# Optimization experiments

Hardware: AMD Instinct MI355X
Metric: run time of the kernel (lower is better)

Reference implementation:

```python
import jax, jax.numpy as jnp
import numpy as np

B, S, D, H = 4, 2048, 1024, 16
DK = D // H


def setup_inputs() -> dict:
    key = jax.random.key(0)
    ks = jax.random.split(key, 5)
    scale = 1.0 / np.sqrt(D)
    return {
        "x": jax.random.normal(ks[0], (B, S, D), dtype=jnp.float32),
        "mask": jnp.ones((1, 1, S, S), dtype=bool),
        "Wq": jax.random.normal(ks[1], (D, D), dtype=jnp.float32) * scale,
        "Wk": jax.random.normal(ks[2], (D, D), dtype=jnp.float32) * scale,
        "Wv": jax.random.normal(ks[3], (D, D), dtype=jnp.float32) * scale,
        "Wo": jax.random.normal(ks[4], (D, D), dtype=jnp.float32) * scale,
    }


def reference(x, mask, Wq, Wk, Wv, Wo):
    # nn.Linear(d_model, d_model, bias=False): y = x @ W.T
    q = jnp.einsum('bsd,ed->bse', x, Wq).reshape(B, S, H, DK).transpose(0, 2, 1, 3)
    k = jnp.einsum('bsd,ed->bse', x, Wk).reshape(B, S, H, DK).transpose(0, 2, 1, 3)
    v = jnp.einsum('bsd,ed->bse', x, Wv).reshape(B, S, H, DK).transpose(0, 2, 1, 3)
    # scaled dot-product attention: [B,H,S,S]
    scores = jnp.einsum('bhqd,bhkd->bhqk', q, k) / jnp.sqrt(jnp.float32(DK))
    scores = jnp.where(mask, scores, jnp.float32(-1e9))
    attn = jax.nn.softmax(scores, axis=-1)
    out = jnp.einsum('bhqk,bhkd->bhqd', attn, v)  # [B,H,S,DK]
    out = out.transpose(0, 2, 1, 3).reshape(B, S, D)
    return jnp.einsum('bsd,ed->bse', out, Wo)
```

## Files before the change

### kernel.cpp

```cpp
#include <hip/hip_runtime.h>

typedef __bf16 bf16x8 __attribute__((ext_vector_type(8)));
typedef float f32x4 __attribute__((ext_vector_type(4)));
typedef float f32x16 __attribute__((ext_vector_type(16)));
typedef unsigned short u16;
typedef unsigned short u16x8 __attribute__((ext_vector_type(8)));
typedef unsigned short u16x4 __attribute__((ext_vector_type(4)));
typedef unsigned int u32;
typedef unsigned int u32x4 __attribute__((ext_vector_type(4)));

#define MFMA16(a, b, c) __builtin_amdgcn_mfma_f32_16x16x32_bf16(a, b, c, 0, 0, 0)
#define MFMA32(a, b, c) __builtin_amdgcn_mfma_f32_32x32x16_bf16(a, b, c, 0, 0, 0)

#if defined(__has_builtin)
#if __has_builtin(__builtin_amdgcn_exp2f)
#define EXP2(x) __builtin_amdgcn_exp2f(x)
#endif
#endif
#ifndef EXP2
#define EXP2(x) exp2f(x)
#endif

constexpr int NB = 4, NH = 16, SEQ = 2048, DM = 1024, DKH = 64;
constexpr int MTOT = NB * SEQ;
constexpr size_t QKV_ELEMS = (size_t)MTOT * DM;
constexpr size_t W_ELEMS = (size_t)DM * DM;
constexpr float QSCALE = 0.125f * 1.44269504088896340736f;

__device__ __forceinline__ int swz(int row, int col, int rowlen) {
  return (row * rowlen + col) ^ ((row & 7) << 3);
}

__device__ __forceinline__ void gload16(const u16* g, u16* l) {
  __builtin_amdgcn_global_load_lds(
      (const __attribute__((address_space(1))) void*)g,
      (__attribute__((address_space(3))) void*)l, 16, 0, 0);
}

__device__ __forceinline__ u32 cvtpk(float lo, float hi) {
  u32 r;
  asm("v_cvt_pk_bf16_f32 %0, %1, %2" : "=v"(r) : "v"(lo), "v"(hi));
  return r;
}
__device__ __forceinline__ void plswap(u32& a, u32& b) {
  asm volatile("v_permlane32_swap_b32 %0, %1" : "+v"(a), "+v"(b));
}

__global__ __launch_bounds__(256) void convert_bf16(
    const float* __restrict__ X, const float* __restrict__ Wq,
    const float* __restrict__ Wk, const float* __restrict__ Wv,
    const float* __restrict__ Wo, u16* __restrict__ Xb,
    u16* __restrict__ Wqb, u16* __restrict__ Wkb, u16* __restrict__ Wvb,
    u16* __restrict__ Wob) {
  const int bid = blockIdx.x;
  const float* src;
  u16* dst;
  size_t base;
  if (bid < 4096) {
    src = X; dst = Xb; base = (size_t)bid * 2048;
  } else {
    const int t = (bid - 4096) >> 9, r = (bid - 4096) & 511;
    src = (t == 0) ? Wq : (t == 1) ? Wk : (t == 2) ? Wv : Wo;
    dst = (t == 0) ? Wqb : (t == 1) ? Wkb : (t == 2) ? Wvb : Wob;
    base = (size_t)r * 2048;
  }
  const size_t e = base + (size_t)threadIdx.x * 8;
  const float4 a = *reinterpret_cast<const float4*>(src + e);
  const float4 b = *reinterpret_cast<const float4*>(src + e + 4);
  bf16x8 v;
  v[0] = (__bf16)a.x; v[1] = (__bf16)a.y; v[2] = (__bf16)a.z; v[3] = (__bf16)a.w;
  v[4] = (__bf16)b.x; v[5] = (__bf16)b.y; v[6] = (__bf16)b.z; v[7] = (__bf16)b.w;
  *reinterpret_cast<bf16x8*>(dst + e) = v;
}

template <int MODE>
__global__ __launch_bounds__(256) void gemm_bt(
    const u16* __restrict__ A, const u16* __restrict__ B,
    u16* __restrict__ Yz, float* __restrict__ Out) {
  constexpr int BM = 128, BK = 64, NT = DM / BK;
  __shared__ __align__(16) u16 As[2][BM * BK];
  __shared__ __align__(16) u16 Bs[2][BM * BK];

  const int tid = threadIdx.x;
  const int lane = tid & 63, w = tid >> 6;
  const int ln = lane & 15, lg = lane >> 4;
  const int wr = (w >> 1) * 64, wc = (w & 1) * 64;
  const int m0 = blockIdx.x * BM, n0 = blockIdx.y * BM;

  const int srow = tid >> 3;
  const int sgg = (tid & 7) ^ (srow & 7);
  const size_t aoff = (size_t)(m0 + srow) * DM + sgg * 8;
  const size_t boff = (size_t)(n0 + srow) * DM + sgg * 8;
  const int lbase = w * 512;

  f32x4 acc[4][4];
#pragma unroll
  for (int i = 0; i < 4; ++i)
#pragma unroll
    for (int j = 0; j < 4; ++j) acc[i][j] = (f32x4){0.f, 0.f, 0.f, 0.f};

  auto stage = [&](int bsel, int k0) {
#pragma unroll
    for (int c = 0; c < 4; ++c) {
      gload16(A + aoff + (size_t)c * 32 * DM + k0, &As[bsel][c * 2048 + lbase]);
      gload16(B + boff + (size_t)c * 32 * DM + k0, &Bs[bsel][c * 2048 + lbase]);
    }
  };

  stage(0, 0);
  __syncthreads();

  int buf = 0;
  for (int t = 0; t < NT; ++t) {
    if (t + 1 < NT) stage(buf ^ 1, (t + 1) * BK);
#pragma unroll
    for (int kc = 0; kc < 2; ++kc) {
      bf16x8 af[4], bfr[4];
#pragma unroll
      for (int i = 0; i < 4; ++i)
        af[i] = *reinterpret_cast<const bf16x8*>(
            &As[buf][swz(wr + i * 16 + ln, kc * 32 + lg * 8, BK)]);
#pragma unroll
      for (int j = 0; j < 4; ++j)
        bfr[j] = *reinterpret_cast<const bf16x8*>(
            &Bs[buf][swz(wc + j * 16 + ln, kc * 32 + lg * 8, BK)]);
      if constexpr (MODE == 2) {
#pragma unroll
        for (int i = 0; i < 4; ++i)
#pragma unroll
          for (int j = 0; j < 4; ++j) acc[i][j] = MFMA16(af[i], bfr[j], acc[i][j]);
      } else {
#pragma unroll
        for (int i = 0; i < 4; ++i)
#pragma unroll
          for (int j = 0; j < 4; ++j) acc[i][j] = MFMA16(bfr[j], af[i], acc[i][j]);
      }
    }
    __syncthreads();
    buf ^= 1;
  }

  if constexpr (MODE == 3) {
#pragma unroll
    for (int i = 0; i < 4; ++i) {
      const int m = m0 + wr + i * 16 + ln;
#pragma unroll
      for (int j = 0; j < 4; ++j) {
        const int nb = n0 + wc + j * 16 + lg * 4;
        float4 v = {acc[i][j][0], acc[i][j][1], acc[i][j][2], acc[i][j][3]};
        *reinterpret_cast<float4*>(&Out[(size_t)m * DM + nb]) = v;
      }
    }
  } else if constexpr (MODE == 2) {
#pragma unroll
    for (int i = 0; i < 4; ++i) {
      const int mB = m0 + wr + i * 16 + lg * 4;
      const int bb = mB >> 11, s0 = mB & (SEQ - 1);
#pragma unroll
      for (int j = 0; j < 4; ++j) {
        const int n = n0 + wc + j * 16 + ln;
        const int h = n >> 6, dk = n & 63;
        u16x4 ov;
#pragma unroll
        for (int r = 0; r < 4; ++r)
          ov[r] = __builtin_bit_cast(u16, (__bf16)acc[i][j][r]);
        *reinterpret_cast<u16x4*>(
            &Yz[(((size_t)(bb * NH + h)) * DKH + dk) * SEQ + s0]) = ov;
      }
    }
  } else {
    const float sc = (MODE == 0) ? QSCALE : 1.0f;
#pragma unroll
    for (int i = 0; i < 4; ++i) {
      const int m = m0 + wr + i * 16 + ln;
      const int bb = m >> 11, s = m & (SEQ - 1);
#pragma unroll
      for (int j = 0; j < 4; ++j) {
        const int nb = n0 + wc + j * 16 + lg * 4;
        const int h = nb >> 6, dk0 = nb & 63;
        u16x4 ov;
#pragma unroll
        for (int r = 0; r < 4; ++r)
          ov[r] = __builtin_bit_cast(u16, (__bf16)(acc[i][j][r] * sc));
        *reinterpret_cast<u16x4*>(
            &Yz[(((size_t)(bb * NH + h)) * SEQ + s) * DKH + dk0]) = ov;
      }
    }
  }
}

__global__ __launch_bounds__(256, 4) void attn_fwd(
    const u16* __restrict__ Qg, const u16* __restrict__ Kg,
    const u16* __restrict__ Vg, u16* __restrict__ Og) {
  constexpr int KVB = 64, NT = SEQ / KVB;
  const int bid = blockIdx.x;
  const int xcd = bid & 7, grp = bid >> 3;
  const int bh = xcd * 8 + (grp >> 4), qt = grp & 15;
  const int b = bh >> 4, h = bh & 15;
  const int tid = threadIdx.x, lane = tid & 63, wv = tid >> 6;
  const int l31 = lane & 31, hi = lane >> 5;
  const size_t hoff = (size_t)bh * SEQ * DKH;
  const u16* __restrict__ Qh = Qg + hoff;
  const u16* __restrict__ Kh = Kg + hoff;
  const u16* __restrict__ Vth = Vg + hoff;

  __shared__ __align__(16) u16 Ks[2][KVB * DKH];
  __shared__ __align__(16) u16 Vs[2][DKH * KVB];

  const int qbase = qt * 128 + wv * 32;

  bf16x8 qf[4];
#pragma unroll
  for (int c = 0; c < 4; ++c)
    qf[c] = *reinterpret_cast<const bf16x8*>(
        Qh + (size_t)(qbase + l31) * DKH + c * 16 + hi * 8);

  float mrow = -1e30f, lr = 0.f;
  f32x16 ot[2];
#pragma unroll
  for (int ds = 0; ds < 2; ++ds)
#pragma unroll
    for (int i = 0; i < 16; ++i) ot[ds][i] = 0.f;

  const int srow = tid >> 3;
  const int sg = (tid & 7) ^ (srow & 7);
  auto stage = [&](int bsel, int kv0) {
#pragma unroll
    for (int c = 0; c < 2; ++c) {
      gload16(Kh + (size_t)(kv0 + c * 32 + srow) * DKH + sg * 8,
              &Ks[bsel][(c * 256 + wv * 64) * 8]);
      gload16(Vth + (size_t)(c * 32 + srow) * SEQ + kv0 + sg * 8,
              &Vs[bsel][(c * 256 + wv * 64) * 8]);
    }
  };

  stage(0, 0);
  __syncthreads();

  int buf = 0;
  for (int t = 0; t < NT; ++t) {
    if (t + 1 < NT) stage(buf ^ 1, (t + 1) * KVB);
    const u16* ksb = Ks[buf];
    const u16* vsb = Vs[buf];

    f32x16 sf[2];
#pragma unroll
    for (int ks = 0; ks < 2; ++ks)
#pragma unroll
      for (int i = 0; i < 16; ++i) sf[ks][i] = 0.f;

    __builtin_amdgcn_s_setprio(1);
#pragma unroll
    for (int ks = 0; ks < 2; ++ks)
#pragma unroll
      for (int c = 0; c < 4; ++c) {
        bf16x8 ka = *reinterpret_cast<const bf16x8*>(
            &ksb[swz(ks * 32 + l31, c * 16 + hi * 8, DKH)]);
        sf[ks] = MFMA32(ka, qf[c], sf[ks]);
      }
    __builtin_amdgcn_s_setprio(0);

    float pm;
    {
      float t16[16];
#pragma unroll
      for (int i = 0; i < 16; ++i) t16[i] = fmaxf(sf[0][i], sf[1][i]);
      float t8[8];
#pragma unroll
      for (int i = 0; i < 8; ++i) t8[i] = fmaxf(t16[i], t16[i + 8]);
      float t4[4];
#pragma unroll
      for (int i = 0; i < 4; ++i) t4[i] = fmaxf(t8[i], t8[i + 4]);
      pm = fmaxf(fmaxf(t4[0], t4[1]), fmaxf(t4[2], t4[3]));
      pm = fmaxf(pm, __shfl_xor(pm, 32));
    }
    if (__any(pm > mrow + 8.f)) {
      const float mn = fmaxf(mrow, pm);
      const float corr = EXP2(mrow - mn);
      mrow = mn;
      lr *= corr;
#pragma unroll
      for (int ds = 0; ds < 2; ++ds)
#pragma unroll
        for (int i = 0; i < 16; ++i) ot[ds][i] *= corr;
    }
    {
      float ls = 0.f;
#pragma unroll
      for (int ks = 0; ks < 2; ++ks)
#pragma unroll
        for (int i = 0; i < 16; ++i) {
          const float p = EXP2(sf[ks][i] - mrow);
          sf[ks][i] = p;
          ls += p;
        }
      ls += __shfl_xor(ls, 32);
      lr += ls;
    }

#pragma unroll
    for (int ks = 0; ks < 2; ++ks) {
#pragma unroll
      for (int hk = 0; hk < 2; ++hk) {
        u32 wA0 = cvtpk(sf[ks][8 * hk + 0], sf[ks][8 * hk + 1]);
        u32 wA1 = cvtpk(sf[ks][8 * hk + 2], sf[ks][8 * hk + 3]);
        u32 wB0 = cvtpk(sf[ks][8 * hk + 4], sf[ks][8 * hk + 5]);
        u32 wB1 = cvtpk(sf[ks][8 * hk + 6], sf[ks][8 * hk + 7]);
        plswap(wA0, wB0);
        plswap(wA1, wB1);
        u32x4 pw;
        pw[0] = wA0; pw[1] = wA1; pw[2] = wB0; pw[3] = wB1;
        const bf16x8 pb = __builtin_bit_cast(bf16x8, pw);
        const int kc = ks * 2 + hk;
        __builtin_amdgcn_s_setprio(1);
#pragma unroll
        for (int ds = 0; ds < 2; ++ds) {
          bf16x8 va = *reinterpret_cast<const bf16x8*>(
              &vsb[swz(ds * 32 + l31, kc * 16 + hi * 8, KVB)]);
          ot[ds] = MFMA32(va, pb, ot[ds]);
        }
        __builtin_amdgcn_s_setprio(0);
      }
    }

    __syncthreads();
    buf ^= 1;
  }

  const float inv = 1.f / lr;
  const int q = qbase + l31;
#pragma unroll
  for (int ds = 0; ds < 2; ++ds)
#pragma unroll
    for (int blk = 0; blk < 4; ++blk) {
      u16x4 ov;
#pragma unroll
      for (int r = 0; r < 4; ++r)
        ov[r] = __builtin_bit_cast(u16, (__bf16)(ot[ds][blk * 4 + r] * inv));
      const int d0 = ds * 32 + blk * 8 + hi * 4;
      *reinterpret_cast<u16x4*>(
          &Og[((size_t)(b * SEQ + q)) * DM + h * DKH + d0]) = ov;
    }
}

extern "C" void kernel_launch(void* const* d_in, const int* in_sizes, int n_in,
                              void* d_out, int out_size, void* d_ws, size_t ws_size,
                              hipStream_t stream) {
  const float* x  = (const float*)d_in[0];
  const float* Wq = (const float*)d_in[2];
  const float* Wk = (const float*)d_in[3];
  const float* Wv = (const float*)d_in[4];
  const float* Wo = (const float*)d_in[5];
  float* out = (float*)d_out;

  u16* Xb  = (u16*)d_ws;
  u16* Wqb = Xb + QKV_ELEMS;
  u16* Wkb = Wqb + W_ELEMS;
  u16* Wvb = Wkb + W_ELEMS;
  u16* Wob = Wvb + W_ELEMS;
  u16* Kb  = Wob + W_ELEMS;
  u16* Vtb = Kb + QKV_ELEMS;
  u16* Qb  = (u16*)d_out;
  u16* Obuf = Xb;

  convert_bf16<<<6144, 256, 0, stream>>>(x, Wq, Wk, Wv, Wo,
                                         Xb, Wqb, Wkb, Wvb, Wob);
  gemm_bt<0><<<dim3(MTOT / 128, DM / 128), 256, 0, stream>>>(Xb, Wqb, Qb, nullptr);
  gemm_bt<1><<<dim3(MTOT / 128, DM / 128), 256, 0, stream>>>(Xb, Wkb, Kb, nullptr);
  gemm_bt<2><<<dim3(MTOT / 128, DM / 128), 256, 0, stream>>>(Xb, Wvb, Vtb, nullptr);
  attn_fwd<<<dim3(NB * NH * 16), 256, 0, stream>>>(Qb, Kb, Vtb, Obuf);
  gemm_bt<3><<<dim3(MTOT / 128, DM / 128), 256, 0, stream>>>(Obuf, Wob, nullptr, out);
}
```

Before: 216.3 us.

## Merge QKV GEMMs into one launch and rework attention staging and row sums

Fuses the three Q/K/V projection launches into a single grid whose y dimension selects the weight and output, so one launch can fill more of the GPU and the per-launch tail is paid once. The attention kernel now stages K and V tiles in an MFMA-fragment-native layout, so each lane reads its operand directly at lane*8 instead of through swizzled row indexing. It also computes the softmax row sum with an extra MFMA against a ones vector instead of per-lane adds and a shuffle. The extra MFMA per PV step adds matrix-core work, and the runtime mode branch in the fused GEMM adds some divergence overhead.

```diff
diff --git a/kernel.cpp b/kernel.cpp
--- a/kernel.cpp
+++ b/kernel.cpp
@@ -73,10 +73,130 @@
   *reinterpret_cast<bf16x8*>(dst + e) = v;
 }
 
-template <int MODE>
-__global__ __launch_bounds__(256) void gemm_bt(
+__global__ __launch_bounds__(256) void gemm_qkv(
+    const u16* __restrict__ A, const u16* __restrict__ Wqb,
+    const u16* __restrict__ Wkb, const u16* __restrict__ Wvb,
+    u16* __restrict__ Qb, u16* __restrict__ Kb, u16* __restrict__ Vtb) {
+  constexpr int BM = 128, BK = 64, NT = DM / BK;
+  __shared__ __align__(16) u16 As[2][BM * BK];
+  __shared__ __align__(16) u16 Bs[2][BM * BK];
+
+  const int mode = blockIdx.y >> 3;
+  const u16* B = (mode == 0) ? Wqb : (mode == 1) ? Wkb : Wvb;
+  u16* Yz = (mode == 0) ? Qb : (mode == 1) ? Kb : Vtb;
+
+  const int tid = threadIdx.x;
+  const int lane = tid & 63, w = tid >> 6;
+  const int ln = lane & 15, lg = lane >> 4;
+  const int wr = (w >> 1) * 64, wc = (w & 1) * 64;
+  const int m0 = blockIdx.x * BM, n0 = (blockIdx.y & 7) * BM;
+
+  const int srow = tid >> 3;
+  const int sgg = (tid & 7) ^ (srow & 7);
+  const size_t aoff = (size_t)(m0 + srow) * DM + sgg * 8;
+  const size_t boff = (size_t)(n0 + srow) * DM + sgg * 8;
+  const int lbase = w * 512;
+
+  f32x4 acc[4][4];
+#pragma unroll
+  for (int i = 0; i < 4; ++i)
+#pragma unroll
+    for (int j = 0; j < 4; ++j) acc[i][j] = (f32x4){0.f, 0.f, 0.f, 0.f};
+
+  auto stage = [&](int bsel, int k0) {
+#pragma unroll
+    for (int c = 0; c < 4; ++c) {
+      gload16(A + aoff + (size_t)c * 32 * DM + k0, &As[bsel][c * 2048 + lbase]);
+      gload16(B + boff + (size_t)c * 32 * DM + k0, &Bs[bsel][c * 2048 + lbase]);
+    }
+  };
+
+  stage(0, 0);
+  __syncthreads();
+
+  int buf = 0;
+  for (int t = 0; t < NT; ++t) {
+    if (t + 1 < NT) stage(buf ^ 1, (t + 1) * BK);
+    if (mode == 2) {
+#pragma unroll
+      for (int kc = 0; kc < 2; ++kc) {
+        bf16x8 af[4], bfr[4];
+#pragma unroll
+        for (int i = 0; i < 4; ++i)
+          af[i] = *reinterpret_cast<const bf16x8*>(
+              &As[buf][swz(wr + i * 16 + ln, kc * 32 + lg * 8, BK)]);
+#pragma unroll
+        for (int j = 0; j < 4; ++j)
+          bfr[j] = *reinterpret_cast<const bf16x8*>(
+              &Bs[buf][swz(wc + j * 16 + ln, kc * 32 + lg * 8, BK)]);
+#pragma unroll
+        for (int i = 0; i < 4; ++i)
+#pragma unroll
+          for (int j = 0; j < 4; ++j) acc[i][j] = MFMA16(af[i], bfr[j], acc[i][j]);
+      }
+    } else {
+#pragma unroll
+      for (int kc = 0; kc < 2; ++kc) {
+        bf16x8 af[4], bfr[4];
+#pragma unroll
+        for (int i = 0; i < 4; ++i)
+          af[i] = *reinterpret_cast<const bf16x8*>(
+              &As[buf][swz(wr + i * 16 + ln, kc * 32 + lg * 8, BK)]);
+#pragma unroll
+        for (int j = 0; j < 4; ++j)
+          bfr[j] = *reinterpret_cast<const bf16x8*>(
+              &Bs[buf][swz(wc + j * 16 + ln, kc * 32 + lg * 8, BK)]);
+#pragma unroll
+        for (int i = 0; i < 4; ++i)
+#pragma unroll
+          for (int j = 0; j < 4; ++j) acc[i][j] = MFMA16(bfr[j], af[i], acc[i][j]);
+      }
+    }
+    __syncthreads();
+    buf ^= 1;
+  }
+
+  if (mode == 2) {
+#pragma unroll
+    for (int i = 0; i < 4; ++i) {
+      const int mB = m0 + wr + i * 16 + lg * 4;
+      const int bb = mB >> 11, s0 = mB & (SEQ - 1);
+#pragma unroll
+      for (int j = 0; j < 4; ++j) {
+        const int n = n0 + wc + j * 16 + ln;
+        const int h = n >> 6, dk = n & 63;
+        u16x4 ov;
+#pragma unroll
+        for (int r = 0; r < 4; ++r)
+          ov[r] = __builtin_bit_cast(u16, (__bf16)acc[i][j][r]);
+        *reinterpret_cast<u16x4*>(
+            &Yz[(((size_t)(bb * NH + h)) * DKH + dk) * SEQ + s0]) = ov;
+      }
+    }
+  } else {
+    const float sc = (mode == 0) ? QSCALE : 1.0f;
+#pragma unroll
+    for (int i = 0; i < 4; ++i) {
+      const int m = m0 + wr + i * 16 + ln;
+      const int bb = m >> 11, s = m & (SEQ - 1);
+#pragma unroll
+      for (int j = 0; j < 4; ++j) {
+        const int nb = n0 + wc + j * 16 + lg * 4;
+        const int h = nb >> 6, dk0 = nb & 63;
+        u16x4 ov;
+#pragma unroll
+        for (int r = 0; r < 4; ++r)
+          ov[r] = __builtin_bit_cast(u16, (__bf16)(acc[i][j][r] * sc));
+        *reinterpret_cast<u16x4*>(
+            &Yz[(((size_t)(bb * NH + h)) * SEQ + s) * DKH + dk0]) = ov;
+      }
+    }
+  }
+}
+
+__global__ __launch_bounds__(256) void gemm_out(
     const u16* __restrict__ A, const u16* __restrict__ B,
-    u16* __restrict__ Yz, float* __restrict__ Out) {
+    float* __restrict__ Out) {
   constexpr int BM = 128, BK = 64, NT = DM / BK;
   __shared__ __align__(16) u16 As[2][BM * BK];
   __shared__ __align__(16) u16 Bs[2][BM * BK];
@@ -124,67 +244,23 @@
       for (int j = 0; j < 4; ++j)
         bfr[j] = *reinterpret_cast<const bf16x8*>(
             &Bs[buf][swz(wc + j * 16 + ln, kc * 32 + lg * 8, BK)]);
-      if constexpr (MODE == 2) {
-#pragma unroll
-        for (int i = 0; i < 4; ++i)
-#pragma unroll
-          for (int j = 0; j < 4; ++j) acc[i][j] = MFMA16(af[i], bfr[j], acc[i][j]);
-      } else {
-#pragma unroll
-        for (int i = 0; i < 4; ++i)
-#pragma unroll
-          for (int j = 0; j < 4; ++j) acc[i][j] = MFMA16(bfr[j], af[i], acc[i][j]);
-      }
+#pragma unroll
+      for (int i = 0; i < 4; ++i)
+#pragma unroll
+        for (int j = 0; j < 4; ++j) acc[i][j] = MFMA16(bfr[j], af[i], acc[i][j]);
     }
     __syncthreads();
     buf ^= 1;
   }
 
-  if constexpr (MODE == 3) {
-#pragma unroll
-    for (int i = 0; i < 4; ++i) {
-      const int m = m0 + wr + i * 16 + ln;
-#pragma unroll
-      for (int j = 0; j < 4; ++j) {
-        const int nb = n0 + wc + j * 16 + lg * 4;
-        float4 v = {acc[i][j][0], acc[i][j][1], acc[i][j][2], acc[i][j][3]};
-        *reinterpret_cast<float4*>(&Out[(size_t)m * DM + nb]) = v;
-      }
-    }
-  } else if constexpr (MODE == 2) {
-#pragma unroll
-    for (int i = 0; i < 4; ++i) {
-      const int mB = m0 + wr + i * 16 + lg * 4;
-      const int bb = mB >> 11, s0 = mB & (SEQ - 1);
-#pragma unroll
-      for (int j = 0; j < 4; ++j) {
-        const int n = n0 + wc + j * 16 + ln;
-        const int h = n >> 6, dk = n & 63;
-        u16x4 ov;
-#pragma unroll
-        for (int r = 0; r < 4; ++r)
-          ov[r] = __builtin_bit_cast(u16, (__bf16)acc[i][j][r]);
-        *reinterpret_cast<u16x4*>(
-            &Yz[(((size_t)(bb * NH + h)) * DKH + dk) * SEQ + s0]) = ov;
-      }
-    }
-  } else {
-    const float sc = (MODE == 0) ? QSCALE : 1.0f;
-#pragma unroll
-    for (int i = 0; i < 4; ++i) {
-      const int m = m0 + wr + i * 16 + ln;
-      const int bb = m >> 11, s = m & (SEQ - 1);
-#pragma unroll
-      for (int j = 0; j < 4; ++j) {
-        const int nb = n0 + wc + j * 16 + lg * 4;
-        const int h = nb >> 6, dk0 = nb & 63;
-        u16x4 ov;
-#pragma unroll
-        for (int r = 0; r < 4; ++r)
-          ov[r] = __builtin_bit_cast(u16, (__bf16)(acc[i][j][r] * sc));
-        *reinterpret_cast<u16x4*>(
-            &Yz[(((size_t)(bb * NH + h)) * SEQ + s) * DKH + dk0]) = ov;
-      }
+#pragma unroll
+  for (int i = 0; i < 4; ++i) {
+    const int m = m0 + wr + i * 16 + ln;
+#pragma unroll
+    for (int j = 0; j < 4; ++j) {
+      const int nb = n0 + wc + j * 16 + lg * 4;
+      float4 v = {acc[i][j][0], acc[i][j][1], acc[i][j][2], acc[i][j][3]};
+      *reinterpret_cast<float4*>(&Out[(size_t)m * DM + nb]) = v;
     }
   }
 }
@@ -204,8 +280,8 @@
   const u16* __restrict__ Kh = Kg + hoff;
   const u16* __restrict__ Vth = Vg + hoff;
 
-  __shared__ __align__(16) u16 Ks[2][KVB * DKH];
-  __shared__ __align__(16) u16 Vs[2][DKH * KVB];
+  __shared__ __align__(16) u16 Ks[2][8 * 512];
+  __shared__ __align__(16) u16 Vs[2][8 * 512];
 
   const int qbase = qt * 128 + wv * 32;
 
@@ -215,23 +291,25 @@
     qf[c] = *reinterpret_cast<const bf16x8*>(
         Qh + (size_t)(qbase + l31) * DKH + c * 16 + hi * 8);
 
-  float mrow = -1e30f, lr = 0.f;
-  f32x16 ot[2];
-#pragma unroll
-  for (int ds = 0; ds < 2; ++ds)
-#pragma unroll
-    for (int i = 0; i < 16; ++i) ot[ds][i] = 0.f;
-
-  const int srow = tid >> 3;
-  const int sg = (tid & 7) ^ (srow & 7);
+  bf16x8 ones;
+#pragma unroll
+  for (int e = 0; e < 8; ++e) ones[e] = (__bf16)1.0f;
+
+  float mrow = -1e30f;
+  f32x16 ot[2], lacc;
+#pragma unroll
+  for (int i = 0; i < 16; ++i) { ot[0][i] = 0.f; ot[1][i] = 0.f; lacc[i] = 0.f; }
+
+  const u16* sK0 = Kh + (size_t)l31 * DKH + wv * 16 + hi * 8;
+  const u16* sK1 = sK0 + 32 * DKH;
+  const u16* sV0 = Vth + (size_t)l31 * SEQ + wv * 16 + hi * 8;
+  const u16* sV1 = sV0 + (size_t)32 * SEQ;
+
   auto stage = [&](int bsel, int kv0) {
-#pragma unroll
-    for (int c = 0; c < 2; ++c) {
-      gload16(Kh + (size_t)(kv0 + c * 32 + srow) * DKH + sg * 8,
-              &Ks[bsel][(c * 256 + wv * 64) * 8]);
-      gload16(Vth + (size_t)(c * 32 + srow) * SEQ + kv0 + sg * 8,
-              &Vs[bsel][(c * 256 + wv * 64) * 8]);
-    }
+    gload16(sK0 + (size_t)kv0 * DKH, &Ks[bsel][wv * 512]);
+    gload16(sK1 + (size_t)kv0 * DKH, &Ks[bsel][(wv + 4) * 512]);
+    gload16(sV0 + kv0, &Vs[bsel][wv * 512]);
+    gload16(sV1 + kv0, &Vs[bsel][(wv + 4) * 512]);
   };
 
   stage(0, 0);
@@ -245,9 +323,7 @@
 
     f32x16 sf[2];
 #pragma unroll
-    for (int ks = 0; ks < 2; ++ks)
-#pragma unroll
-      for (int i = 0; i < 16; ++i) sf[ks][i] = 0.f;
+    for (int i = 0; i < 16; ++i) { sf[0][i] = 0.f; sf[1][i] = 0.f; }
 
     __builtin_amdgcn_s_setprio(1);
 #pragma unroll
@@ -255,48 +331,36 @@
 #pragma unroll
       for (int c = 0; c < 4; ++c) {
         bf16x8 ka = *reinterpret_cast<const bf16x8*>(
-            &ksb[swz(ks * 32 + l31, c * 16 + hi * 8, DKH)]);
+            &ksb[(ks * 4 + c) * 512 + lane * 8]);
         sf[ks] = MFMA32(ka, qf[c], sf[ks]);
       }
     __builtin_amdgcn_s_setprio(0);
 
-    float pm;
-    {
-      float t16[16];
-#pragma unroll
-      for (int i = 0; i < 16; ++i) t16[i] = fmaxf(sf[0][i], sf[1][i]);
-      float t8[8];
-#pragma unroll
-      for (int i = 0; i < 8; ++i) t8[i] = fmaxf(t16[i], t16[i + 8]);
-      float t4[4];
-#pragma unroll
-      for (int i = 0; i < 4; ++i) t4[i] = fmaxf(t8[i], t8[i + 4]);
-      pm = fmaxf(fmaxf(t4[0], t4[1]), fmaxf(t4[2], t4[3]));
-      pm = fmaxf(pm, __shfl_xor(pm, 32));
-    }
+    float t8[8];
+#pragma unroll
+    for (int i = 0; i < 8; ++i)
+      t8[i] = fmaxf(fmaxf(sf[0][i], sf[0][i + 8]),
+                    fmaxf(sf[1][i], sf[1][i + 8]));
+    float ta = fmaxf(fmaxf(t8[0], t8[1]), t8[2]);
+    float tb = fmaxf(fmaxf(t8[3], t8[4]), t8[5]);
+    float tc = fmaxf(fmaxf(t8[6], t8[7]), ta);
+    float pm = fmaxf(tb, tc);
+    pm = fmaxf(pm, __shfl_xor(pm, 32));
+
     if (__any(pm > mrow + 8.f)) {
       const float mn = fmaxf(mrow, pm);
       const float corr = EXP2(mrow - mn);
       mrow = mn;
-      lr *= corr;
-#pragma unroll
-      for (int ds = 0; ds < 2; ++ds)
-#pragma unroll
-        for (int i = 0; i < 16; ++i) ot[ds][i] *= corr;
-    }
-    {
-      float ls = 0.f;
-#pragma unroll
-      for (int ks = 0; ks < 2; ++ks)
-#pragma unroll
-        for (int i = 0; i < 16; ++i) {
-          const float p = EXP2(sf[ks][i] - mrow);
-          sf[ks][i] = p;
-          ls += p;
-        }
-      ls += __shfl_xor(ls, 32);
-      lr += ls;
-    }
+      lacc *= corr;
+      ot[0] *= corr;
+      ot[1] *= corr;
+    }
+    sf[0] = sf[0] - mrow;
+    sf[1] = sf[1] - mrow;
+#pragma unroll
+    for (int ks = 0; ks < 2; ++ks)
+#pragma unroll
+      for (int i = 0; i < 16; ++i) sf[ks][i] = EXP2(sf[ks][i]);
 
 #pragma unroll
     for (int ks = 0; ks < 2; ++ks) {
@@ -313,12 +377,13 @@
         const bf16x8 pb = __builtin_bit_cast(bf16x8, pw);
         const int kc = ks * 2 + hk;
         __builtin_amdgcn_s_setprio(1);
-#pragma unroll
-        for (int ds = 0; ds < 2; ++ds) {
-          bf16x8 va = *reinterpret_cast<const bf16x8*>(
-              &vsb[swz(ds * 32 + l31, kc * 16 + hi * 8, KVB)]);
-          ot[ds] = MFMA32(va, pb, ot[ds]);
-        }
+        bf16x8 va0 = *reinterpret_cast<const bf16x8*>(
+            &vsb[(0 * 4 + kc) * 512 + lane * 8]);
+        bf16x8 va1 = *reinterpret_cast<const bf16x8*>(
+            &vsb[(1 * 4 + kc) * 512 + lane * 8]);
+        ot[0] = MFMA32(va0, pb, ot[0]);
+        ot[1] = MFMA32(va1, pb, ot[1]);
+        lacc = MFMA32(ones, pb, lacc);
         __builtin_amdgcn_s_setprio(0);
       }
     }
@@ -327,7 +392,7 @@
     buf ^= 1;
   }
 
-  const float inv = 1.f / lr;
+  const float inv = 1.f / lacc[0];
   const int q = qbase + l31;
 #pragma unroll
   for (int ds = 0; ds < 2; ++ds)
@@ -365,9 +430,8 @@
 
   convert_bf16<<<6144, 256, 0, stream>>>(x, Wq, Wk, Wv, Wo,
                                          Xb, Wqb, Wkb, Wvb, Wob);
-  gemm_bt<0><<<dim3(MTOT / 128, DM / 128), 256, 0, stream>>>(Xb, Wqb, Qb, nullptr);
-  gemm_bt<1><<<dim3(MTOT / 128, DM / 128), 256, 0, stream>>>(Xb, Wkb, Kb, nullptr);
-  gemm_bt<2><<<dim3(MTOT / 128, DM / 128), 256, 0, stream>>>(Xb, Wvb, Vtb, nullptr);
+  gemm_qkv<<<dim3(MTOT / 128, 24), 256, 0, stream>>>(Xb, Wqb, Wkb, Wvb,
+                                                     Qb, Kb, Vtb);
   attn_fwd<<<dim3(NB * NH * 16), 256, 0, stream>>>(Qb, Kb, Vtb, Obuf);
-  gemm_bt<3><<<dim3(MTOT / 128, DM / 128), 256, 0, stream>>>(Obuf, Wob, nullptr, out);
-}
+  gemm_out<<<dim3(MTOT / 128, DM / 128), 256, 0, stream>>>(Obuf, Wob, out);
+}
```

Result: faster. 208.8 us (-3.5%).
